# Kernel optimization log

Measured on AMD Instinct MI355X. Metric: run time of the kernel, lower is better.

## Reference

```python
import jax, jax.numpy as jnp
import numpy as np

B, T, FIN, D = 8, 512, 256, 128


def setup_inputs() -> dict:
    key = jax.random.key(0)
    ks = jax.random.split(key, 12)
    s = lambda fan_in: 1.0 / np.sqrt(fan_in)
    return {
        "x": jax.random.normal(ks[0], (B, T, FIN), jnp.float32),
        "S0": jnp.zeros((B, 1, D, D), jnp.float32),
        "Z0": jnp.zeros((B, 1, D), jnp.float32),
        "gamma": jnp.ones((FIN,), jnp.float32),
        "beta": jnp.zeros((FIN,), jnp.float32),
        "Wk": jax.random.normal(ks[1], (FIN, D), jnp.float32) * s(FIN),
        "Wq": jax.random.normal(ks[2], (FIN, D), jnp.float32) * s(FIN),
        "Wv": jax.random.normal(ks[3], (FIN, D), jnp.float32) * s(FIN),
        "W1": jax.random.normal(ks[4], (D, D), jnp.float32) * s(D),
        "b1": jnp.zeros((D,), jnp.float32),
        "W2": jax.random.normal(ks[5], (D, D), jnp.float32) * s(D),
        "b2": jnp.zeros((D,), jnp.float32),
        "Ws": jax.random.normal(ks[6], (FIN, D), jnp.float32) * s(FIN),
        "bs": jnp.zeros((D,), jnp.float32),
    }


def reference(x, S0, Z0, gamma, beta, Wk, Wq, Wv, W1, b1, W2, b2, Ws, bs):
    CLAMP = 1e20
    # LayerNorm over feature dim
    mu = jnp.mean(x, axis=-1, keepdims=True)
    var = jnp.var(x, axis=-1, keepdims=True)
    xn = (x - mu) / jnp.sqrt(var + 1e-5) * gamma + beta
    # phi(x) = elu(x) + 1
    K = jax.nn.elu(xn @ Wk) + 1.0  # [B,T,D]
    Q = jax.nn.elu(xn @ Wq) + 1.0  # [B,T,D]
    V = xn @ Wv                     # [B,T,D]
    # outer-product state recurrence via cumsum (faithful to original)
    outer = jnp.einsum('bti,btj->btij', K, V)            # [B,T,D,D]
    S = jnp.clip(jnp.cumsum(outer, axis=1), -CLAMP, CLAMP) + S0  # [B,T,D,D]
    Z = jnp.clip(jnp.cumsum(K, axis=1), -CLAMP, CLAMP) + Z0      # [B,T,D]
    numerator = jnp.einsum('bti,btil->btl', Q, S)        # [B,T,D]
    denominator = jnp.einsum('bti,bti->bt', Q, Z)[..., None] + 1e-5
    out = numerator / denominator
    # FFN: relu(relu(out W1 + b1) W2 + b2)
    out = jax.nn.relu(jax.nn.relu(out @ W1 + b1) @ W2 + b2)
    # residual shortcut from normed input
    out = out + xn @ Ws + bs
    S_out = S.reshape(B, T, D * D)
    return out, S_out, Z
```

## Files before the change

kernel.cpp:

```cpp
#include <hip/hip_runtime.h>


constexpr int BB = 8, TT = 512, FIN_ = 256, DD = 128;
constexpr int NROW = BB * TT;
constexpr int CLEN = 64, NCH = 8;
constexpr float CLAMPV = 1e20f;

typedef float f4v __attribute__((ext_vector_type(4)));

__global__ __launch_bounds__(256) void gemm_qkvs(
    const float* __restrict__ x,
    const float* __restrict__ gamma, const float* __restrict__ beta,
    const float* __restrict__ Wk, const float* __restrict__ Wq,
    const float* __restrict__ Wv, const float* __restrict__ Ws,
    const float* __restrict__ bs,
    float* __restrict__ Kb, float* __restrict__ Qb,
    float* __restrict__ Vb, float* __restrict__ Rb)
{
  int ct = blockIdx.x, rt = blockIdx.y;
  int mat = ct >> 1, cb = (ct & 1) * 64;
  const float* W = (mat == 0) ? Wk : (mat == 1) ? Wq : (mat == 2) ? Wv : Ws;
  float* Ob      = (mat == 0) ? Kb : (mat == 1) ? Qb : (mat == 2) ? Vb : Rb;
  __shared__ float As[16][64];
  __shared__ float Bs[16][64];
  __shared__ float mu_s[64], rs_s[64];
  int tid = threadIdx.x;
  {
    int row = tid >> 2, q = tid & 3;
    const float* xr = &x[(rt * 64 + row) * FIN_ + q * 64];
    float sum = 0.f, sq = 0.f;
#pragma unroll
    for (int u = 0; u < 16; u++) {
      float4 v = *(const float4*)&xr[u * 4];
      sum += v.x + v.y + v.z + v.w;
      sq  += v.x * v.x + v.y * v.y + v.z * v.z + v.w * v.w;
    }
    sum += __shfl_xor(sum, 1); sq += __shfl_xor(sq, 1);
    sum += __shfl_xor(sum, 2); sq += __shfl_xor(sq, 2);
    if (q == 0) {
      float mu = sum * (1.0f / FIN_);
      float var = sq * (1.0f / FIN_) - mu * mu;
      mu_s[row] = mu;
      rs_s[row] = rsqrtf(var + 1e-5f);
    }
  }
  __syncthreads();
  int tn = tid & 15, tm = tid >> 4;
  int lm = tid >> 2, lq = tid & 3;
  int lk = tid >> 4, ln4 = (tid & 15) * 4;
  float acc[4][4] = {};
  float mu = mu_s[lm], rs = rs_s[lm];
  for (int k0 = 0; k0 < FIN_; k0 += 16) {
    float4 av = *(const float4*)&x[(rt * 64 + lm) * FIN_ + k0 + lq * 4];
    float4 g  = *(const float4*)&gamma[k0 + lq * 4];
    float4 be = *(const float4*)&beta[k0 + lq * 4];
    As[lq * 4 + 0][lm] = (av.x - mu) * rs * g.x + be.x;
    As[lq * 4 + 1][lm] = (av.y - mu) * rs * g.y + be.y;
    As[lq * 4 + 2][lm] = (av.z - mu) * rs * g.z + be.z;
    As[lq * 4 + 3][lm] = (av.w - mu) * rs * g.w + be.w;
    *(float4*)&Bs[lk][ln4] = *(const float4*)&W[(k0 + lk) * DD + cb + ln4];
    __syncthreads();
#pragma unroll
    for (int k = 0; k < 16; k++) {
      float4 a = *(const float4*)&As[k][tm * 4];
      float4 b = *(const float4*)&Bs[k][tn * 4];
      float ar[4] = {a.x, a.y, a.z, a.w};
      float br[4] = {b.x, b.y, b.z, b.w};
#pragma unroll
      for (int i = 0; i < 4; i++)
#pragma unroll
        for (int j = 0; j < 4; j++) acc[i][j] += ar[i] * br[j];
    }
    __syncthreads();
  }
#pragma unroll
  for (int i = 0; i < 4; i++) {
    int row = rt * 64 + tm * 4 + i;
    int col = cb + tn * 4;
    float vals[4];
#pragma unroll
    for (int j = 0; j < 4; j++) {
      float v = acc[i][j];
      if (mat <= 1) v = (v > 0.f) ? v + 1.f : expf(v);
      else if (mat == 3) v += bs[col + j];
      vals[j] = v;
    }
    float4 o = make_float4(vals[0], vals[1], vals[2], vals[3]);
    *(float4*)&Ob[row * DD + col] = o;
  }
}

__global__ __launch_bounds__(256) void prefix_kernel(
    const float* __restrict__ Kb, const float* __restrict__ Vb,
    const float* __restrict__ S0, const float* __restrict__ Z0,
    float* __restrict__ prefS, float* __restrict__ prefz)
{
  int jt = blockIdx.x, it = blockIdx.y, b = blockIdx.z;
  int i0 = it * 16, j0 = jt * 32;
  __shared__ float Ks[CLEN][16];
  __shared__ float Vs[CLEN][32];
  int tid = threadIdx.x;
  int il = tid >> 4, jl = tid & 15;
  float2 s0v = *(const float2*)&S0[b * DD * DD + (i0 + il) * DD + j0 + jl * 2];
  float acc0 = 0.f, acc1 = 0.f;
  float zacc = 0.f;
  float z0v = (jt == 0 && tid < 16) ? Z0[b * DD + i0 + tid] : 0.f;
  for (int c = 0; c < NCH; c++) {
    const float* Kc = Kb + (b * TT + c * CLEN) * DD;
    const float* Vc = Vb + (b * TT + c * CLEN) * DD;
    {
      int t = tid >> 2, i4 = (tid & 3) * 4;
      *(float4*)&Ks[t][i4] = *(const float4*)&Kc[t * DD + i0 + i4];
    }
#pragma unroll
    for (int u = 0; u < 2; u++) {
      int idx = u * 256 + tid;
      int t = idx >> 3, j4 = (idx & 7) * 4;
      *(float4*)&Vs[t][j4] = *(const float4*)&Vc[t * DD + j0 + j4];
    }
    __syncthreads();
    float2 op = make_float2(acc0 + s0v.x, acc1 + s0v.y);
    *(float2*)&prefS[(size_t)(b * NCH + c) * DD * DD + (i0 + il) * DD + j0 + jl * 2] = op;
    if (jt == 0 && tid < 16)
      prefz[(b * NCH + c) * DD + i0 + tid] = zacc + z0v;
#pragma unroll 8
    for (int t = 0; t < CLEN; t++) {
      float k = Ks[t][il];
      float2 v2 = *(const float2*)&Vs[t][jl * 2];
      acc0 += k * v2.x;
      acc1 += k * v2.y;
    }
    if (jt == 0 && tid < 16) {
      float z = 0.f;
#pragma unroll 8
      for (int t = 0; t < CLEN; t++) z += Ks[t][tid];
      zacc += z;
    }
    __syncthreads();
  }
}

union MegaSmem {
  struct {
    float KsT[DD][CLEN + 2];
    float Qs[8][132];
    float sc[8][CLEN + 2];
    float zeff[DD];
    float den[8];
    float As[8][132];
    float H1[8][132];
  } a;
  struct {
    float Vs[CLEN][DD];
    float Ksm[CLEN][8];
  } s;
};

__global__ __launch_bounds__(256) void mega_kernel(
    const float* __restrict__ Kb, const float* __restrict__ Qb,
    const float* __restrict__ Vb, const float* __restrict__ prefS,
    const float* __restrict__ prefz, const float* __restrict__ Rb,
    const float* __restrict__ W1, const float* __restrict__ b1,
    const float* __restrict__ W2, const float* __restrict__ b2,
    float* __restrict__ Zout, float* __restrict__ out_main,
    float* __restrict__ Sout)
{
  __shared__ MegaSmem sm;
  int c = blockIdx.y, b = blockIdx.z, tid = threadIdx.x;
  const float* Kc = Kb + (b * TT + c * CLEN) * DD;
  const float* Vc = Vb + (b * TT + c * CLEN) * DD;

  if (blockIdx.x >= 8) {
    int it = blockIdx.x - 8;
    int i0 = it * 8;
#pragma unroll
    for (int u = 0; u < 8; u++) {
      int idx = u * 256 + tid;
      int t = idx >> 5, c4 = (idx & 31) * 4;
      *(float4*)&sm.s.Vs[t][c4] = *(const float4*)&Vc[t * DD + c4];
    }
#pragma unroll
    for (int u = 0; u < 2; u++) {
      int idx = u * 256 + tid;
      int t = idx >> 3, r = idx & 7;
      sm.s.Ksm[t][r] = Kc[t * DD + i0 + r];
    }
    __syncthreads();
    int irow = tid >> 5, jq = tid & 31;
    int j = jq * 4;
    float4 pref = *(const float4*)&prefS[(size_t)(b * NCH + c) * DD * DD + (i0 + irow) * DD + j];
    float4 acc = make_float4(0.f, 0.f, 0.f, 0.f);
    float* So = Sout + (size_t)(b * TT + c * CLEN) * (DD * DD) + (i0 + irow) * DD + j;
#pragma unroll 4
    for (int t = 0; t < CLEN; t++) {
      float4 v4 = *(const float4*)&sm.s.Vs[t][j];
      float kk = sm.s.Ksm[t][irow];
      acc.x += kk * v4.x; acc.y += kk * v4.y;
      acc.z += kk * v4.z; acc.w += kk * v4.w;
      f4v o4;
      o4.x = fminf(fmaxf(pref.x + acc.x, -CLAMPV), CLAMPV);
      o4.y = fminf(fmaxf(pref.y + acc.y, -CLAMPV), CLAMPV);
      o4.z = fminf(fmaxf(pref.z + acc.z, -CLAMPV), CLAMPV);
      o4.w = fminf(fmaxf(pref.w + acc.w, -CLAMPV), CLAMPV);
      __builtin_nontemporal_store(o4, (f4v*)&So[(size_t)t * (DD * DD)]);
    }
    return;
  }

  int sub = blockIdx.x;
  int t0 = sub * 8;
  int tlim = t0 + 8;
  const float* Qc = Qb + (b * TT + c * CLEN) * DD;
  for (int idx = tid; idx < tlim * 32; idx += 256) {
    int t = idx >> 5, c4 = (idx & 31) * 4;
    float4 v = *(const float4*)&Kc[t * DD + c4];
    sm.a.KsT[c4 + 0][t] = v.x; sm.a.KsT[c4 + 1][t] = v.y;
    sm.a.KsT[c4 + 2][t] = v.z; sm.a.KsT[c4 + 3][t] = v.w;
  }
  {
    int r = tid >> 5, c4 = (tid & 31) * 4;
    float4 q = *(const float4*)&Qc[(t0 + r) * DD + c4];
    *(float4*)&sm.a.Qs[r][c4] = q;
  }
  if (tid < DD) sm.a.zeff[tid] = prefz[(b * NCH + c) * DD + tid];
  __syncthreads();
  {
    int tm = tid >> 5, tn = tid & 31;
    int tau0 = tn * 2;
    if (tau0 < tlim) {
      float s0 = 0.f, s1 = 0.f;
#pragma unroll 8
      for (int k = 0; k < DD; k++) {
        float q = sm.a.Qs[tm][k];
        float2 kk = *(const float2*)&sm.a.KsT[k][tau0];
        s0 += q * kk.x;
        s1 += q * kk.y;
      }
      int t = t0 + tm;
      sm.a.sc[tm][tau0]     = (tau0     <= t) ? s0 : 0.f;
      sm.a.sc[tm][tau0 + 1] = (tau0 + 1 <= t) ? s1 : 0.f;
    }
  }
  __syncthreads();
  if (tid < 8) {
    int t = t0 + tid;
    float d = 0.f;
    for (int tau = 0; tau <= t; tau++) d += sm.a.sc[tid][tau];
    float dz = 0.f;
#pragma unroll 8
    for (int k = 0; k < DD; k++) dz += sm.a.Qs[tid][k] * sm.a.zeff[k];
    sm.a.den[tid] = d + dz + 1e-5f;
  }
  __syncthreads();
  int tl = tid & 31, r = tid >> 5;
  int l0 = tl * 4;
  {
    float n0[4] = {};
#pragma unroll 4
    for (int tau = 0; tau < tlim; tau++) {
      float4 v4 = *(const float4*)&Vc[tau * DD + l0];
      float s = sm.a.sc[r][tau];
      n0[0] += s * v4.x; n0[1] += s * v4.y; n0[2] += s * v4.z; n0[3] += s * v4.w;
    }
    const float* P = prefS + (size_t)(b * NCH + c) * DD * DD;
#pragma unroll 4
    for (int i = 0; i < DD; i++) {
      float4 p4 = *(const float4*)&P[i * DD + l0];
      float q = sm.a.Qs[r][i];
      n0[0] += q * p4.x; n0[1] += q * p4.y; n0[2] += q * p4.z; n0[3] += q * p4.w;
    }
    float dd = sm.a.den[r];
    float4 o = make_float4(n0[0] / dd, n0[1] / dd, n0[2] / dd, n0[3] / dd);
    *(float4*)&sm.a.As[r][l0] = o;
  }
  if (sub == 7 && tid < DD) {
    int i = tid;
    float a = sm.a.zeff[i];
    for (int t = 0; t < CLEN; t++) {
      a += sm.a.KsT[i][t];
      a = fminf(fmaxf(a, -CLAMPV), CLAMPV);
      __builtin_nontemporal_store(a, &Zout[(size_t)(b * TT + c * CLEN + t) * DD + i]);
    }
  }
  __syncthreads();
  {
    float a1[4] = {};
#pragma unroll 8
    for (int k = 0; k < DD; k++) {
      float4 w = *(const float4*)&W1[k * DD + l0];
      float a = sm.a.As[r][k];
      a1[0] += a * w.x; a1[1] += a * w.y; a1[2] += a * w.z; a1[3] += a * w.w;
    }
    float4 bv = *(const float4*)&b1[l0];
    float4 h;
    h.x = fmaxf(a1[0] + bv.x, 0.f);
    h.y = fmaxf(a1[1] + bv.y, 0.f);
    h.z = fmaxf(a1[2] + bv.z, 0.f);
    h.w = fmaxf(a1[3] + bv.w, 0.f);
    *(float4*)&sm.a.H1[r][l0] = h;
  }
  __syncthreads();
  {
    float a2[4] = {};
#pragma unroll 8
    for (int k = 0; k < DD; k++) {
      float4 w = *(const float4*)&W2[k * DD + l0];
      float a = sm.a.H1[r][k];
      a2[0] += a * w.x; a2[1] += a * w.y; a2[2] += a * w.z; a2[3] += a * w.w;
    }
    int grow = b * TT + c * CLEN + t0 + r;
    float4 b2v = *(const float4*)&b2[l0];
    float4 rv = *(const float4*)&Rb[grow * DD + l0];
    float4 o;
    o.x = fmaxf(a2[0] + b2v.x, 0.f) + rv.x;
    o.y = fmaxf(a2[1] + b2v.y, 0.f) + rv.y;
    o.z = fmaxf(a2[2] + b2v.z, 0.f) + rv.z;
    o.w = fmaxf(a2[3] + b2v.w, 0.f) + rv.w;
    *(float4*)&out_main[grow * DD + l0] = o;
  }
}

extern "C" void kernel_launch(void* const* d_in, const int* in_sizes, int n_in,
                              void* d_out, int out_size, void* d_ws, size_t ws_size,
                              hipStream_t stream)
{
  const float* x     = (const float*)d_in[0];
  const float* S0    = (const float*)d_in[1];
  const float* Z0    = (const float*)d_in[2];
  const float* gamma = (const float*)d_in[3];
  const float* beta  = (const float*)d_in[4];
  const float* Wk    = (const float*)d_in[5];
  const float* Wq    = (const float*)d_in[6];
  const float* Wv    = (const float*)d_in[7];
  const float* W1    = (const float*)d_in[8];
  const float* b1    = (const float*)d_in[9];
  const float* W2    = (const float*)d_in[10];
  const float* b2    = (const float*)d_in[11];
  const float* Ws    = (const float*)d_in[12];
  const float* bs    = (const float*)d_in[13];

  float* out_main = (float*)d_out;
  float* Sout = out_main + NROW * DD;
  float* Zout = Sout + (size_t)NROW * DD * DD;

  float* ws_f   = (float*)d_ws;
  float* Kb     = ws_f;
  float* Qb     = Kb + 524288;
  float* Vb     = Qb + 524288;
  float* Rb     = Vb + 524288;
  float* prefS  = Rb + 524288;
  float* prefz  = prefS + 1048576;

  gemm_qkvs<<<dim3(8, 64), 256, 0, stream>>>(x, gamma, beta, Wk, Wq, Wv, Ws, bs,
                                             Kb, Qb, Vb, Rb);
  prefix_kernel<<<dim3(4, 8, BB), 256, 0, stream>>>(Kb, Vb, S0, Z0, prefS, prefz);
  mega_kernel<<<dim3(24, NCH, BB), 256, 0, stream>>>(Kb, Qb, Vb, prefS, prefz, Rb,
                                                     W1, b1, W2, b2,
                                                     Zout, out_main, Sout);
}
```

Before: 381.9 us.

## Double-buffer GEMM and prefix tiles, widen S-writer blocks, parallelize denominator

```diff
diff --git a/kernel.cpp b/kernel.cpp
--- a/kernel.cpp
+++ b/kernel.cpp
@@ -21,8 +21,8 @@
   int mat = ct >> 1, cb = (ct & 1) * 64;
   const float* W = (mat == 0) ? Wk : (mat == 1) ? Wq : (mat == 2) ? Wv : Ws;
   float* Ob      = (mat == 0) ? Kb : (mat == 1) ? Qb : (mat == 2) ? Vb : Rb;
-  __shared__ float As[16][64];
-  __shared__ float Bs[16][64];
+  __shared__ float As[2][16][64];
+  __shared__ float Bs[2][16][64];
   __shared__ float mu_s[64], rs_s[64];
   int tid = threadIdx.x;
   {
@@ -50,20 +50,28 @@
   int lk = tid >> 4, ln4 = (tid & 15) * 4;
   float acc[4][4] = {};
   float mu = mu_s[lm], rs = rs_s[lm];
+  float4 xa = *(const float4*)&x[(rt * 64 + lm) * FIN_ + lq * 4];
+  float4 ga = *(const float4*)&gamma[lq * 4];
+  float4 be = *(const float4*)&beta[lq * 4];
+  float4 wb = *(const float4*)&W[lk * DD + cb + ln4];
+  int cur = 0;
   for (int k0 = 0; k0 < FIN_; k0 += 16) {
-    float4 av = *(const float4*)&x[(rt * 64 + lm) * FIN_ + k0 + lq * 4];
-    float4 g  = *(const float4*)&gamma[k0 + lq * 4];
-    float4 be = *(const float4*)&beta[k0 + lq * 4];
-    As[lq * 4 + 0][lm] = (av.x - mu) * rs * g.x + be.x;
-    As[lq * 4 + 1][lm] = (av.y - mu) * rs * g.y + be.y;
-    As[lq * 4 + 2][lm] = (av.z - mu) * rs * g.z + be.z;
-    As[lq * 4 + 3][lm] = (av.w - mu) * rs * g.w + be.w;
-    *(float4*)&Bs[lk][ln4] = *(const float4*)&W[(k0 + lk) * DD + cb + ln4];
+    As[cur][lq * 4 + 0][lm] = (xa.x - mu) * rs * ga.x + be.x;
+    As[cur][lq * 4 + 1][lm] = (xa.y - mu) * rs * ga.y + be.y;
+    As[cur][lq * 4 + 2][lm] = (xa.z - mu) * rs * ga.z + be.z;
+    As[cur][lq * 4 + 3][lm] = (xa.w - mu) * rs * ga.w + be.w;
+    *(float4*)&Bs[cur][lk][ln4] = wb;
+    if (k0 + 16 < FIN_) {
+      xa = *(const float4*)&x[(rt * 64 + lm) * FIN_ + k0 + 16 + lq * 4];
+      ga = *(const float4*)&gamma[k0 + 16 + lq * 4];
+      be = *(const float4*)&beta[k0 + 16 + lq * 4];
+      wb = *(const float4*)&W[(k0 + 16 + lk) * DD + cb + ln4];
+    }
     __syncthreads();
 #pragma unroll
     for (int k = 0; k < 16; k++) {
-      float4 a = *(const float4*)&As[k][tm * 4];
-      float4 b = *(const float4*)&Bs[k][tn * 4];
+      float4 a = *(const float4*)&As[cur][k][tm * 4];
+      float4 b = *(const float4*)&Bs[cur][k][tn * 4];
       float ar[4] = {a.x, a.y, a.z, a.w};
       float br[4] = {b.x, b.y, b.z, b.w};
 #pragma unroll
@@ -71,7 +79,7 @@
 #pragma unroll
         for (int j = 0; j < 4; j++) acc[i][j] += ar[i] * br[j];
     }
-    __syncthreads();
+    cur ^= 1;
   }
 #pragma unroll
   for (int i = 0; i < 4; i++) {
@@ -85,8 +93,7 @@
       else if (mat == 3) v += bs[col + j];
       vals[j] = v;
     }
-    float4 o = make_float4(vals[0], vals[1], vals[2], vals[3]);
-    *(float4*)&Ob[row * DD + col] = o;
+    *(float4*)&Ob[row * DD + col] = make_float4(vals[0], vals[1], vals[2], vals[3]);
   }
 }
 
@@ -97,46 +104,62 @@
 {
   int jt = blockIdx.x, it = blockIdx.y, b = blockIdx.z;
   int i0 = it * 16, j0 = jt * 32;
-  __shared__ float Ks[CLEN][16];
-  __shared__ float Vs[CLEN][32];
+  __shared__ float Ks[2][CLEN][16];
+  __shared__ float Vs[2][CLEN][32];
   int tid = threadIdx.x;
   int il = tid >> 4, jl = tid & 15;
   float2 s0v = *(const float2*)&S0[b * DD * DD + (i0 + il) * DD + j0 + jl * 2];
   float acc0 = 0.f, acc1 = 0.f;
   float zacc = 0.f;
   float z0v = (jt == 0 && tid < 16) ? Z0[b * DD + i0 + tid] : 0.f;
-  for (int c = 0; c < NCH; c++) {
-    const float* Kc = Kb + (b * TT + c * CLEN) * DD;
-    const float* Vc = Vb + (b * TT + c * CLEN) * DD;
-    {
-      int t = tid >> 2, i4 = (tid & 3) * 4;
-      *(float4*)&Ks[t][i4] = *(const float4*)&Kc[t * DD + i0 + i4];
-    }
+  {
+    const float* Kc = Kb + (b * TT) * DD;
+    const float* Vc = Vb + (b * TT) * DD;
+    int t = tid >> 2, i4 = (tid & 3) * 4;
+    *(float4*)&Ks[0][t][i4] = *(const float4*)&Kc[t * DD + i0 + i4];
 #pragma unroll
     for (int u = 0; u < 2; u++) {
       int idx = u * 256 + tid;
-      int t = idx >> 3, j4 = (idx & 7) * 4;
-      *(float4*)&Vs[t][j4] = *(const float4*)&Vc[t * DD + j0 + j4];
-    }
+      int tv = idx >> 3, j4 = (idx & 7) * 4;
+      *(float4*)&Vs[0][tv][j4] = *(const float4*)&Vc[tv * DD + j0 + j4];
+    }
+  }
+  int cur = 0;
+  for (int c = 0; c < NCH; c++) {
     __syncthreads();
+    float4 kq, vq0, vq1;
+    if (c + 1 < NCH) {
+      const float* Kc = Kb + (b * TT + (c + 1) * CLEN) * DD;
+      const float* Vc = Vb + (b * TT + (c + 1) * CLEN) * DD;
+      kq  = *(const float4*)&Kc[(tid >> 2) * DD + i0 + (tid & 3) * 4];
+      vq0 = *(const float4*)&Vc[(tid >> 3) * DD + j0 + (tid & 7) * 4];
+      int idx = 256 + tid;
+      vq1 = *(const float4*)&Vc[(idx >> 3) * DD + j0 + (idx & 7) * 4];
+    }
     float2 op = make_float2(acc0 + s0v.x, acc1 + s0v.y);
     *(float2*)&prefS[(size_t)(b * NCH + c) * DD * DD + (i0 + il) * DD + j0 + jl * 2] = op;
     if (jt == 0 && tid < 16)
       prefz[(b * NCH + c) * DD + i0 + tid] = zacc + z0v;
 #pragma unroll 8
     for (int t = 0; t < CLEN; t++) {
-      float k = Ks[t][il];
-      float2 v2 = *(const float2*)&Vs[t][jl * 2];
+      float k = Ks[cur][t][il];
+      float2 v2 = *(const float2*)&Vs[cur][t][jl * 2];
       acc0 += k * v2.x;
       acc1 += k * v2.y;
     }
     if (jt == 0 && tid < 16) {
       float z = 0.f;
 #pragma unroll 8
-      for (int t = 0; t < CLEN; t++) z += Ks[t][tid];
+      for (int t = 0; t < CLEN; t++) z += Ks[cur][t][tid];
       zacc += z;
     }
-    __syncthreads();
+    if (c + 1 < NCH) {
+      *(float4*)&Ks[cur ^ 1][tid >> 2][(tid & 3) * 4] = kq;
+      *(float4*)&Vs[cur ^ 1][tid >> 3][(tid & 7) * 4] = vq0;
+      int idx = 256 + tid;
+      *(float4*)&Vs[cur ^ 1][idx >> 3][(idx & 7) * 4] = vq1;
+    }
+    cur ^= 1;
   }
 }
 
@@ -152,7 +175,7 @@
   } a;
   struct {
     float Vs[CLEN][DD];
-    float Ksm[CLEN][8];
+    float Ksm[CLEN][16];
   } s;
 };
 
@@ -171,8 +194,7 @@
   const float* Vc = Vb + (b * TT + c * CLEN) * DD;
 
   if (blockIdx.x >= 8) {
-    int it = blockIdx.x - 8;
-    int i0 = it * 8;
+    int i0 = (blockIdx.x - 8) * 16;
 #pragma unroll
     for (int u = 0; u < 8; u++) {
       int idx = u * 256 + tid;
@@ -180,29 +202,42 @@
       *(float4*)&sm.s.Vs[t][c4] = *(const float4*)&Vc[t * DD + c4];
     }
 #pragma unroll
-    for (int u = 0; u < 2; u++) {
+    for (int u = 0; u < 4; u++) {
       int idx = u * 256 + tid;
-      int t = idx >> 3, r = idx & 7;
+      int t = idx >> 4, r = idx & 15;
       sm.s.Ksm[t][r] = Kc[t * DD + i0 + r];
     }
     __syncthreads();
     int irow = tid >> 5, jq = tid & 31;
     int j = jq * 4;
-    float4 pref = *(const float4*)&prefS[(size_t)(b * NCH + c) * DD * DD + (i0 + irow) * DD + j];
-    float4 acc = make_float4(0.f, 0.f, 0.f, 0.f);
-    float* So = Sout + (size_t)(b * TT + c * CLEN) * (DD * DD) + (i0 + irow) * DD + j;
-#pragma unroll 4
+    size_t pbase = (size_t)(b * NCH + c) * DD * DD;
+    float4 prefA = *(const float4*)&prefS[pbase + (i0 + irow) * DD + j];
+    float4 prefB = *(const float4*)&prefS[pbase + (i0 + 8 + irow) * DD + j];
+    float4 accA = make_float4(0.f, 0.f, 0.f, 0.f);
+    float4 accB = make_float4(0.f, 0.f, 0.f, 0.f);
+    float* SoA = Sout + (size_t)(b * TT + c * CLEN) * (DD * DD) + (i0 + irow) * DD + j;
+    float* SoB = SoA + 8 * DD;
+#pragma unroll 2
     for (int t = 0; t < CLEN; t++) {
       float4 v4 = *(const float4*)&sm.s.Vs[t][j];
-      float kk = sm.s.Ksm[t][irow];
-      acc.x += kk * v4.x; acc.y += kk * v4.y;
-      acc.z += kk * v4.z; acc.w += kk * v4.w;
-      f4v o4;
-      o4.x = fminf(fmaxf(pref.x + acc.x, -CLAMPV), CLAMPV);
-      o4.y = fminf(fmaxf(pref.y + acc.y, -CLAMPV), CLAMPV);
-      o4.z = fminf(fmaxf(pref.z + acc.z, -CLAMPV), CLAMPV);
-      o4.w = fminf(fmaxf(pref.w + acc.w, -CLAMPV), CLAMPV);
-      __builtin_nontemporal_store(o4, (f4v*)&So[(size_t)t * (DD * DD)]);
+      float kA = sm.s.Ksm[t][irow];
+      float kB = sm.s.Ksm[t][irow + 8];
+      accA.x += kA * v4.x; accA.y += kA * v4.y;
+      accA.z += kA * v4.z; accA.w += kA * v4.w;
+      f4v oA;
+      oA.x = fminf(fmaxf(prefA.x + accA.x, -CLAMPV), CLAMPV);
+      oA.y = fminf(fmaxf(prefA.y + accA.y, -CLAMPV), CLAMPV);
+      oA.z = fminf(fmaxf(prefA.z + accA.z, -CLAMPV), CLAMPV);
+      oA.w = fminf(fmaxf(prefA.w + accA.w, -CLAMPV), CLAMPV);
+      __builtin_nontemporal_store(oA, (f4v*)&SoA[(size_t)t * (DD * DD)]);
+      accB.x += kB * v4.x; accB.y += kB * v4.y;
+      accB.z += kB * v4.z; accB.w += kB * v4.w;
+      f4v oB;
+      oB.x = fminf(fmaxf(prefB.x + accB.x, -CLAMPV), CLAMPV);
+      oB.y = fminf(fmaxf(prefB.y + accB.y, -CLAMPV), CLAMPV);
+      oB.z = fminf(fmaxf(prefB.z + accB.z, -CLAMPV), CLAMPV);
+      oB.w = fminf(fmaxf(prefB.w + accB.w, -CLAMPV), CLAMPV);
+      __builtin_nontemporal_store(oB, (f4v*)&SoB[(size_t)t * (DD * DD)]);
     }
     return;
   }
@@ -213,14 +248,13 @@
   const float* Qc = Qb + (b * TT + c * CLEN) * DD;
   for (int idx = tid; idx < tlim * 32; idx += 256) {
     int t = idx >> 5, c4 = (idx & 31) * 4;
-    float4 v = *(const float4*)&Kc[t * DD + c4];
-    sm.a.KsT[c4 + 0][t] = v.x; sm.a.KsT[c4 + 1][t] = v.y;
-    sm.a.KsT[c4 + 2][t] = v.z; sm.a.KsT[c4 + 3][t] = v.w;
+    float4 vv = *(const float4*)&Kc[t * DD + c4];
+    sm.a.KsT[c4 + 0][t] = vv.x; sm.a.KsT[c4 + 1][t] = vv.y;
+    sm.a.KsT[c4 + 2][t] = vv.z; sm.a.KsT[c4 + 3][t] = vv.w;
   }
   {
     int r = tid >> 5, c4 = (tid & 31) * 4;
-    float4 q = *(const float4*)&Qc[(t0 + r) * DD + c4];
-    *(float4*)&sm.a.Qs[r][c4] = q;
+    *(float4*)&sm.a.Qs[r][c4] = *(const float4*)&Qc[(t0 + r) * DD + c4];
   }
   if (tid < DD) sm.a.zeff[tid] = prefz[(b * NCH + c) * DD + tid];
   __syncthreads();
@@ -242,14 +276,16 @@
     }
   }
   __syncthreads();
-  if (tid < 8) {
-    int t = t0 + tid;
-    float d = 0.f;
-    for (int tau = 0; tau <= t; tau++) d += sm.a.sc[tid][tau];
-    float dz = 0.f;
-#pragma unroll 8
-    for (int k = 0; k < DD; k++) dz += sm.a.Qs[tid][k] * sm.a.zeff[k];
-    sm.a.den[tid] = d + dz + 1e-5f;
+  {
+    int r = tid >> 5, g = tid & 31;
+    int t = t0 + r;
+    float p = 0.f;
+    for (int tau = g; tau <= t; tau += 32) p += sm.a.sc[r][tau];
+#pragma unroll 4
+    for (int k = g; k < DD; k += 32) p += sm.a.Qs[r][k] * sm.a.zeff[k];
+#pragma unroll
+    for (int off = 1; off < 32; off <<= 1) p += __shfl_xor(p, off);
+    if (g == 0) sm.a.den[r] = p + 1e-5f;
   }
   __syncthreads();
   int tl = tid & 31, r = tid >> 5;
@@ -270,8 +306,8 @@
       n0[0] += q * p4.x; n0[1] += q * p4.y; n0[2] += q * p4.z; n0[3] += q * p4.w;
     }
     float dd = sm.a.den[r];
-    float4 o = make_float4(n0[0] / dd, n0[1] / dd, n0[2] / dd, n0[3] / dd);
-    *(float4*)&sm.a.As[r][l0] = o;
+    *(float4*)&sm.a.As[r][l0] =
+        make_float4(n0[0] / dd, n0[1] / dd, n0[2] / dd, n0[3] / dd);
   }
   if (sub == 7 && tid < DD) {
     int i = tid;
@@ -354,7 +390,7 @@
   gemm_qkvs<<<dim3(8, 64), 256, 0, stream>>>(x, gamma, beta, Wk, Wq, Wv, Ws, bs,
                                              Kb, Qb, Vb, Rb);
   prefix_kernel<<<dim3(4, 8, BB), 256, 0, stream>>>(Kb, Vb, S0, Z0, prefS, prefz);
-  mega_kernel<<<dim3(24, NCH, BB), 256, 0, stream>>>(Kb, Qb, Vb, prefS, prefz, Rb,
+  mega_kernel<<<dim3(16, NCH, BB), 256, 0, stream>>>(Kb, Qb, Vb, prefS, prefz, Rb,
                                                      W1, b1, W2, b2,
                                                      Zout, out_main, Sout);
 }
```

New measurement: 373.9 us. -2.1%, faster.
